# Kernel optimization log

Measured on AMD Instinct MI355X. Metric: run time of the kernel, lower is better.

The kernel has to match this reference:

```python
import jax, jax.numpy as jnp
import numpy as np

CAT_SIZES = [31360, 6807, 18, 94]
TOTAL = int(sum(CAT_SIZES))          # 38279
EMB = 128
N_FIELDS = len(CAT_SIZES)
D_IN = N_FIELDS * EMB                # 512 (num_features is empty)
MLP_DIMS = [2048, 1024, 512]
B = 16384
OFFSETS = np.concatenate([[0], np.cumsum(CAT_SIZES)[:-1]]).astype(np.int32)


def setup_inputs() -> dict:
    key = jax.random.key(0)
    ks = jax.random.split(key, 20)
    # x holds raw per-field category ids stored as float32 (as the torch model expects)
    cols = [jax.random.randint(ks[i], (B,), 0, s) for i, s in enumerate(CAT_SIZES)]
    x = jnp.stack(cols, axis=1).astype(jnp.float32)

    bias = jnp.zeros((1,), jnp.float32)
    fc = jax.random.uniform(ks[4], (TOTAL, 1), dtype=jnp.float32)          # nn.Parameter(torch.rand)
    emb_table = jax.random.normal(ks[5], (TOTAL, EMB), dtype=jnp.float32)  # nn.Embedding default N(0,1)

    dims = [D_IN] + MLP_DIMS + [1]
    params = {}
    for i in range(len(dims) - 1):
        fan_in = dims[i]
        bound = 1.0 / np.sqrt(fan_in)
        params[f"W{i+1}"] = jax.random.uniform(ks[6 + 2 * i], (dims[i], dims[i + 1]), jnp.float32, -bound, bound)
        params[f"b{i+1}"] = jax.random.uniform(ks[7 + 2 * i], (dims[i + 1],), jnp.float32, -bound, bound)

    return dict(x=x, bias=bias, fc=fc, emb_table=emb_table, **params)


def reference(x, bias, fc, emb_table, W1, b1, W2, b2, W3, b3, W4, b4):
    cat = x.astype(jnp.int32)                       # [B, F] raw per-field ids
    b = cat.shape[0]

    # embedding lookup with RAW (un-offset) ids, faithful to the original code
    embed_x = emb_table[cat].reshape(b, -1)          # [B, F*EMB]

    # one_hot(offset ids) @ fc  ==  sum_f fc[offset ids]  (offset ranges disjoint)
    gidx = cat + jnp.asarray(OFFSETS)                # [B, F] global ids
    lin = jnp.sum(fc[gidx, 0], axis=1)               # [B]
    fm_y = bias + lin                                # [B]

    # FM term: embed_x is 2-D, so sum over dim=1 collapses features;
    # the keepdim sum over dim=-1 then collapses the BATCH dim to shape (1,)
    # (a quirk of the original code that we reproduce exactly)
    square_of_sum = jnp.sum(embed_x, axis=1) ** 2    # [B]
    sum_of_square = jnp.sum(embed_x ** 2, axis=1)    # [B]
    fm_y = fm_y + 0.5 * jnp.sum(square_of_sum - sum_of_square, axis=-1, keepdims=True)  # [B]
    fm_y = fm_y[:, None]                             # [B,1]

    # MLP (eval mode: dropout is identity)
    h = embed_x
    for W, bb in ((W1, b1), (W2, b2), (W3, b3)):
        h = jax.nn.relu(h @ W + bb)
    mlp_y = h @ W4 + b4                              # [B,1]

    return jax.nn.sigmoid(fm_y + mlp_y)              # [B,1]
```

## Files before the change

kernel.cpp:

```cpp
#include <hip/hip_runtime.h>
#include <hip/hip_fp8.h>
#include <cstdint>


typedef float f32x4 __attribute__((ext_vector_type(4)));
typedef int i32x4 __attribute__((ext_vector_type(4)));
typedef int i32x8 __attribute__((ext_vector_type(8)));

#define GLOAD16(gptr, lptr)                                                \
  __builtin_amdgcn_global_load_lds(                                        \
      (const __attribute__((address_space(1))) void*)(gptr),               \
      (__attribute__((address_space(3))) void*)(lptr), 16, 0, 0)

__device__ inline uint32_t f2fp4(float v) {
  uint32_t s = (__float_as_uint(v) >> 31) << 3;
  float a = fabsf(v);
  uint32_t m;
  if (a < 0.25f) m = 0;
  else if (a < 0.75f) m = 1;
  else if (a < 1.25f) m = 2;
  else if (a < 1.75f) m = 3;
  else if (a < 2.5f)  m = 4;
  else if (a < 3.5f)  m = 5;
  else if (a < 5.0f)  m = 6;
  else m = 7;
  return s | m;
}

static constexpr size_t OFF_LIN  = 0;
static constexpr size_t OFF_PART = 65536;
static constexpr size_t OFF_ACC  = 98304;
static constexpr size_t OFF_EMB  = 262144;
static constexpr size_t OFF_H1   = OFF_EMB + 8388608ull;
static constexpr size_t OFF_H2   = OFF_H1 + 33554432ull;
static constexpr size_t OFF_W1T  = OFF_H2 + 16777216ull;
static constexpr size_t OFF_W2T  = OFF_W1T + 524288ull;
static constexpr size_t OFF_W3T  = OFF_W2T + 1048576ull;

__global__ void prep(const float* __restrict__ W1, const float* __restrict__ W2,
                     const float* __restrict__ W3, uint8_t* __restrict__ W1T,
                     uint8_t* __restrict__ W2T, uint8_t* __restrict__ W3T,
                     const float* __restrict__ x, const float* __restrict__ fc,
                     const float* __restrict__ emb, uint8_t* __restrict__ ebf,
                     float* __restrict__ lin, float* __restrict__ partials,
                     float* __restrict__ dotacc) {
  __shared__ __align__(16) float smem[32 * 33];
  int blk = blockIdx.x;
  int tid = threadIdx.x;
  if (blk < 3584) {
    const float* W;
    uint8_t* WT;
    int K, N, bx, by;
    if (blk < 1024) {
      W = W1; WT = W1T; K = 512; N = 2048; bx = blk & 63; by = blk >> 6;
    } else if (blk < 3072) {
      int t = blk - 1024;
      W = W2; WT = W2T; K = 2048; N = 1024; bx = t & 31; by = t >> 5;
    } else {
      int t = blk - 3072;
      W = W3; WT = W3T; K = 1024; N = 512; bx = t & 15; by = t >> 4;
    }
    int tx = tid & 31, ty = tid >> 5;
    int n0 = bx * 32, k0 = by * 32;
#pragma unroll
    for (int i = ty; i < 32; i += 8)
      smem[i * 33 + tx] = W[(size_t)(k0 + i) * N + n0 + tx];
    __syncthreads();
    if (tx < 16) {
#pragma unroll
      for (int i = ty; i < 32; i += 8) {
        uint32_t lo = f2fp4(smem[(2 * tx) * 33 + i] * 128.f);
        uint32_t hi = f2fp4(smem[(2 * tx + 1) * 33 + i] * 128.f);
        WT[(size_t)(n0 + i) * (K >> 1) + (k0 >> 1) + tx] =
            (uint8_t)(lo | (hi << 4));
      }
    }
  } else if (blk < 7680) {
    int gb = blk - 3584;
    int wv = tid >> 6, lane = tid & 63;
    int b = gb * 4 + wv;
    int f = lane >> 4;
    int idx = (int)x[b * 4 + f];
    const float* row = emb + (size_t)idx * 128 + (lane & 15) * 8;
    float4 v0 = ((const float4*)row)[0];
    float4 v1 = ((const float4*)row)[1];
    float s = v0.x + v0.y + v0.z + v0.w + v1.x + v1.y + v1.z + v1.w;
    float q = v0.x * v0.x + v0.y * v0.y + v0.z * v0.z + v0.w * v0.w +
              v1.x * v1.x + v1.y * v1.y + v1.z * v1.z + v1.w * v1.w;

    int lo = 0, hi = 0;
    lo = __builtin_amdgcn_cvt_pk_fp8_f32(v0.x, v0.y, lo, false);
    lo = __builtin_amdgcn_cvt_pk_fp8_f32(v0.z, v0.w, lo, true);
    hi = __builtin_amdgcn_cvt_pk_fp8_f32(v1.x, v1.y, hi, false);
    hi = __builtin_amdgcn_cvt_pk_fp8_f32(v1.z, v1.w, hi, true);
    int2 pk = make_int2(lo, hi);
    *(int2*)(ebf + (size_t)b * 512 + lane * 8) = pk;

    float lp = 0.f;
    if ((lane & 15) == 0) {
      int off = (f == 1) ? 31360 : (f == 2) ? 38167 : (f == 3) ? 38185 : 0;
      lp = fc[idx + off];
    }
#pragma unroll
    for (int m = 32; m; m >>= 1) {
      s += __shfl_xor(s, m);
      q += __shfl_xor(q, m);
      lp += __shfl_xor(lp, m);
    }
    float* pt = smem;
    if (lane == 0) {
      lin[b] = lp;
      pt[wv] = s * s - q;
    }
    __syncthreads();
    if (tid == 0) partials[gb] = pt[0] + pt[1] + pt[2] + pt[3];
  } else {
    int zb = blk - 7680;
    ((float4*)dotacc)[zb * 256 + tid] = make_float4(0.f, 0.f, 0.f, 0.f);
  }
}

__global__ __launch_bounds__(256) void gemm_mx_relu(
    const uint8_t* __restrict__ A, const uint8_t* __restrict__ BT,
    const float* __restrict__ bias, uint8_t* __restrict__ C, int K, int N,
    int GX) {
  __shared__ __align__(16) uint8_t As[128][256];
  __shared__ __align__(16) uint8_t Bs[128][128];
  int bid = blockIdx.x;
  int by = (bid & 7) + ((bid >> 3) / GX) * 8;
  int bx = (bid >> 3) & (GX - 1);
  int tid = threadIdx.x;
  int wv = tid >> 6, lane = tid & 63;
  int m0 = by * 128, n0 = bx * 128;
  int mw = (wv >> 1) * 64, nw = (wv & 1) * 64;
  int ml = lane & 15, kg = lane >> 4;
  int Kb2 = K >> 1;
  int arow = lane >> 4;
  int brow = lane >> 3;
  int bcol = ((lane & 7) ^ brow) * 16;

  f32x4 acc[4][4];
#pragma unroll
  for (int i = 0; i < 4; ++i)
#pragma unroll
    for (int j = 0; j < 4; ++j) acc[i][j] = (f32x4){0.f, 0.f, 0.f, 0.f};

  for (int kt = 0; kt < K; kt += 256) {
#pragma unroll
    for (int r = 0; r < 8; ++r) {
      int g = r * 4 + wv;
      int trow = 4 * g + arow;
      int acol = ((lane & 15) ^ (trow & 15)) * 16;
      const uint8_t* ga = A + (size_t)(m0 + trow) * K + kt + acol;
      GLOAD16(ga, &As[4 * g][0]);
    }
#pragma unroll
    for (int r = 0; r < 4; ++r) {
      int g = r * 4 + wv;
      const uint8_t* gb =
          BT + (size_t)(n0 + 8 * g + brow) * Kb2 + (kt >> 1) + bcol;
      GLOAD16(gb, &Bs[8 * g][0]);
    }
    __syncthreads();

    i32x4 z = (i32x4){0, 0, 0, 0};
#pragma unroll
    for (int j = 0; j < 2; ++j) {
      int c0 = 8 * j + 2 * kg;
      int pa0 = (c0 ^ ml) * 16;
      int pa1 = ((c0 + 1) ^ ml) * 16;
      int pb = ((4 * j + kg) ^ (ml & 7)) * 16;
      i32x8 af[4], bfr[4];
#pragma unroll
      for (int t = 0; t < 4; ++t) {
        int ra = mw + t * 16 + ml;
        i32x4 a0 = *(const i32x4*)&As[ra][pa0];
        i32x4 a1 = *(const i32x4*)&As[ra][pa1];
        af[t] = __builtin_shufflevector(a0, a1, 0, 1, 2, 3, 4, 5, 6, 7);
        i32x4 vb = *(const i32x4*)&Bs[nw + t * 16 + ml][pb];
        bfr[t] = __builtin_shufflevector(vb, z, 0, 1, 2, 3, 4, 5, 6, 7);
      }
#pragma unroll
      for (int mt = 0; mt < 4; ++mt)
#pragma unroll
        for (int nt = 0; nt < 4; ++nt)
          acc[mt][nt] = __builtin_amdgcn_mfma_scale_f32_16x16x128_f8f6f4(
              af[mt], bfr[nt], acc[mt][nt],
               0,  4,
              0, 0x7F7F7F7F, 0, 0x78787878);
    }
    __syncthreads();
  }

  int rbase = kg * 4;
#pragma unroll
  for (int nt = 0; nt < 4; ++nt) {
    int col = n0 + nw + nt * 16 + ml;
    float bv = bias[col];
#pragma unroll
    for (int mt = 0; mt < 4; ++mt) {
      int row = m0 + mw + mt * 16 + rbase;
      float v0 = acc[mt][nt][0] + bv, v1 = acc[mt][nt][1] + bv;
      float v2 = acc[mt][nt][2] + bv, v3 = acc[mt][nt][3] + bv;
      v0 = v0 > 0.f ? v0 : 0.f;
      v1 = v1 > 0.f ? v1 : 0.f;
      v2 = v2 > 0.f ? v2 : 0.f;
      v3 = v3 > 0.f ? v3 : 0.f;
      int w01 = __builtin_amdgcn_cvt_pk_fp8_f32(v0, v1, 0, false);
      int w23 = __builtin_amdgcn_cvt_pk_fp8_f32(v2, v3, 0, false);
      C[(size_t)(row + 0) * N + col] = (uint8_t)(w01 & 0xFF);
      C[(size_t)(row + 1) * N + col] = (uint8_t)((w01 >> 8) & 0xFF);
      C[(size_t)(row + 2) * N + col] = (uint8_t)(w23 & 0xFF);
      C[(size_t)(row + 3) * N + col] = (uint8_t)((w23 >> 8) & 0xFF);
    }
  }
}

__global__ __launch_bounds__(256) void gemm_mx_dot(
    const uint8_t* __restrict__ A, const uint8_t* __restrict__ BT,
    const float* __restrict__ bias, const float* __restrict__ W4,
    float* __restrict__ dotacc, int K, int N, int GX) {
  __shared__ __align__(16) uint8_t As[128][256];
  __shared__ __align__(16) uint8_t Bs[128][128];
  int bid = blockIdx.x;
  int by = (bid & 7) + ((bid >> 3) / GX) * 8;
  int bx = (bid >> 3) & (GX - 1);
  int tid = threadIdx.x;
  int wv = tid >> 6, lane = tid & 63;
  int m0 = by * 128, n0 = bx * 128;
  int mw = (wv >> 1) * 64, nw = (wv & 1) * 64;
  int ml = lane & 15, kg = lane >> 4;
  int Kb2 = K >> 1;
  int arow = lane >> 4;
  int brow = lane >> 3;
  int bcol = ((lane & 7) ^ brow) * 16;

  f32x4 acc[4][4];
#pragma unroll
  for (int i = 0; i < 4; ++i)
#pragma unroll
    for (int j = 0; j < 4; ++j) acc[i][j] = (f32x4){0.f, 0.f, 0.f, 0.f};

  for (int kt = 0; kt < K; kt += 256) {
#pragma unroll
    for (int r = 0; r < 8; ++r) {
      int g = r * 4 + wv;
      int trow = 4 * g + arow;
      int acol = ((lane & 15) ^ (trow & 15)) * 16;
      const uint8_t* ga = A + (size_t)(m0 + trow) * K + kt + acol;
      GLOAD16(ga, &As[4 * g][0]);
    }
#pragma unroll
    for (int r = 0; r < 4; ++r) {
      int g = r * 4 + wv;
      const uint8_t* gb =
          BT + (size_t)(n0 + 8 * g + brow) * Kb2 + (kt >> 1) + bcol;
      GLOAD16(gb, &Bs[8 * g][0]);
    }
    __syncthreads();

    i32x4 z = (i32x4){0, 0, 0, 0};
#pragma unroll
    for (int j = 0; j < 2; ++j) {
      int c0 = 8 * j + 2 * kg;
      int pa0 = (c0 ^ ml) * 16;
      int pa1 = ((c0 + 1) ^ ml) * 16;
      int pb = ((4 * j + kg) ^ (ml & 7)) * 16;
      i32x8 af[4], bfr[4];
#pragma unroll
      for (int t = 0; t < 4; ++t) {
        int ra = mw + t * 16 + ml;
        i32x4 a0 = *(const i32x4*)&As[ra][pa0];
        i32x4 a1 = *(const i32x4*)&As[ra][pa1];
        af[t] = __builtin_shufflevector(a0, a1, 0, 1, 2, 3, 4, 5, 6, 7);
        i32x4 vb = *(const i32x4*)&Bs[nw + t * 16 + ml][pb];
        bfr[t] = __builtin_shufflevector(vb, z, 0, 1, 2, 3, 4, 5, 6, 7);
      }
#pragma unroll
      for (int mt = 0; mt < 4; ++mt)
#pragma unroll
        for (int nt = 0; nt < 4; ++nt)
          acc[mt][nt] = __builtin_amdgcn_mfma_scale_f32_16x16x128_f8f6f4(
              af[mt], bfr[nt], acc[mt][nt],
              0, 4, 0, 0x7F7F7F7F, 0, 0x78787878);
    }
    __syncthreads();
  }

  float bv[4], w4v[4];
#pragma unroll
  for (int nt = 0; nt < 4; ++nt) {
    int col = n0 + nw + nt * 16 + ml;
    bv[nt] = bias[col];
    w4v[nt] = W4[col];
  }
  int rbase = kg * 4;
#pragma unroll
  for (int mt = 0; mt < 4; ++mt) {
#pragma unroll
    for (int r = 0; r < 4; ++r) {
      float p = 0.f;
#pragma unroll
      for (int nt = 0; nt < 4; ++nt) {
        float v = acc[mt][nt][r] + bv[nt];
        v = v > 0.f ? v : 0.f;
        p += v * w4v[nt];
      }
#pragma unroll
      for (int m = 1; m < 16; m <<= 1) p += __shfl_xor(p, m);
      if (ml == 0)
        atomicAdd(&dotacc[m0 + mw + mt * 16 + rbase + r], p);
    }
  }
}

__global__ void final_out(const float* __restrict__ part,
                          const float* __restrict__ dotacc,
                          const float* __restrict__ lin,
                          const float* __restrict__ bias,
                          const float* __restrict__ b4,
                          float* __restrict__ out) {
  __shared__ float ps[4];
  int tid = threadIdx.x;
  float v = 0.f;
  for (int i = tid; i < 4096; i += 256) v += part[i];
#pragma unroll
  for (int m = 32; m; m >>= 1) v += __shfl_xor(v, m);
  if ((tid & 63) == 0) ps[tid >> 6] = v;
  __syncthreads();
  float S = ps[0] + ps[1] + ps[2] + ps[3];
  int i = blockIdx.x * 256 + tid;
  float z = dotacc[i] + b4[0] + bias[0] + lin[i] + 0.5f * S;
  out[i] = 1.f / (1.f + expf(-z));
}

extern "C" void kernel_launch(void* const* d_in, const int* in_sizes, int n_in,
                              void* d_out, int out_size, void* d_ws,
                              size_t ws_size, hipStream_t stream) {
  const float* x    = (const float*)d_in[0];
  const float* bias = (const float*)d_in[1];
  const float* fc   = (const float*)d_in[2];
  const float* emb  = (const float*)d_in[3];
  const float* W1   = (const float*)d_in[4];
  const float* b1   = (const float*)d_in[5];
  const float* W2   = (const float*)d_in[6];
  const float* b2   = (const float*)d_in[7];
  const float* W3   = (const float*)d_in[8];
  const float* b3   = (const float*)d_in[9];
  const float* W4   = (const float*)d_in[10];
  const float* b4   = (const float*)d_in[11];
  float* out = (float*)d_out;

  char* ws = (char*)d_ws;
  float* lin    = (float*)(ws + OFF_LIN);
  float* part   = (float*)(ws + OFF_PART);
  float* dacc   = (float*)(ws + OFF_ACC);
  uint8_t* EMBb = (uint8_t*)(ws + OFF_EMB);
  uint8_t* H1   = (uint8_t*)(ws + OFF_H1);
  uint8_t* H2   = (uint8_t*)(ws + OFF_H2);
  uint8_t* W1T  = (uint8_t*)(ws + OFF_W1T);
  uint8_t* W2T  = (uint8_t*)(ws + OFF_W2T);
  uint8_t* W3T  = (uint8_t*)(ws + OFF_W3T);

  prep<<<7696, 256, 0, stream>>>(W1, W2, W3, W1T, W2T, W3T, x, fc, emb, EMBb,
                                 lin, part, dacc);

  gemm_mx_relu<<<2048, 256, 0, stream>>>(EMBb, W1T, b1, H1, 512, 2048, 16);
  gemm_mx_relu<<<1024, 256, 0, stream>>>(H1, W2T, b2, H2, 2048, 1024, 8);
  gemm_mx_dot<<<512, 256, 0, stream>>>(H2, W3T, b3, W4, dacc, 1024, 512, 4);

  final_out<<<64, 256, 0, stream>>>(part, dacc, lin, bias, b4, out);
}
```

Before: 177.1 us.

## Double-buffer LDS tiles with K=128 steps in MX GEMM kernels

Both MX-fp8/fp4 GEMM kernels now use two LDS buffers with a K-step of 128 instead of one buffer with a K-step of 256. The next tile is prefetched with global_load_lds while the current one is consumed, using explicit vmcnt waits and raw barriers in place of __syncthreads. MFMA issue is wrapped in s_setprio. The LDS swizzle patterns are redone for the narrower tiles. This targets load latency that the old single-buffer loop exposed, at the cost of more iterations and barriers per K and reliance on exact vmcnt counting.

```diff
diff --git a/kernel.cpp b/kernel.cpp
--- a/kernel.cpp
+++ b/kernel.cpp
@@ -11,6 +11,9 @@
   __builtin_amdgcn_global_load_lds(                                        \
       (const __attribute__((address_space(1))) void*)(gptr),               \
       (__attribute__((address_space(3))) void*)(lptr), 16, 0, 0)
+
+#define BARRIER() asm volatile("s_barrier" ::: "memory")
+#define WAITVM(n) asm volatile("s_waitcnt vmcnt(" #n ")" ::: "memory")
 
 __device__ inline uint32_t f2fp4(float v) {
   uint32_t s = (__float_as_uint(v) >> 31) << 3;
@@ -124,8 +127,8 @@
     const uint8_t* __restrict__ A, const uint8_t* __restrict__ BT,
     const float* __restrict__ bias, uint8_t* __restrict__ C, int K, int N,
     int GX) {
-  __shared__ __align__(16) uint8_t As[128][256];
-  __shared__ __align__(16) uint8_t Bs[128][128];
+  __shared__ __align__(16) uint8_t As[2][128][128];
+  __shared__ __align__(16) uint8_t Bs[2][128][64];
   int bid = blockIdx.x;
   int by = (bid & 7) + ((bid >> 3) / GX) * 8;
   int bx = (bid >> 3) & (GX - 1);
@@ -135,9 +138,11 @@
   int mw = (wv >> 1) * 64, nw = (wv & 1) * 64;
   int ml = lane & 15, kg = lane >> 4;
   int Kb2 = K >> 1;
-  int arow = lane >> 4;
-  int brow = lane >> 3;
-  int bcol = ((lane & 7) ^ brow) * 16;
+
+  int arow = lane >> 3;
+  int acol = ((lane & 7) ^ arow) * 16;
+  int brow = lane >> 2;
+  int bcol = ((lane & 3) ^ ((lane >> 3) & 3)) * 16;
 
   f32x4 acc[4][4];
 #pragma unroll
@@ -145,63 +150,74 @@
 #pragma unroll
     for (int j = 0; j < 4; ++j) acc[i][j] = (f32x4){0.f, 0.f, 0.f, 0.f};
 
-  for (int kt = 0; kt < K; kt += 256) {
-#pragma unroll
-    for (int r = 0; r < 8; ++r) {
-      int g = r * 4 + wv;
-      int trow = 4 * g + arow;
-      int acol = ((lane & 15) ^ (trow & 15)) * 16;
-      const uint8_t* ga = A + (size_t)(m0 + trow) * K + kt + acol;
-      GLOAD16(ga, &As[4 * g][0]);
-    }
+  int nt = K >> 7;
+
+  auto stage = [&](int buf, int kt) {
 #pragma unroll
     for (int r = 0; r < 4; ++r) {
       int g = r * 4 + wv;
+      const uint8_t* ga = A + (size_t)(m0 + 8 * g + arow) * K + kt + acol;
+      GLOAD16(ga, &As[buf][8 * g][0]);
+    }
+#pragma unroll
+    for (int r = 0; r < 2; ++r) {
+      int g = r * 4 + wv;
       const uint8_t* gb =
-          BT + (size_t)(n0 + 8 * g + brow) * Kb2 + (kt >> 1) + bcol;
-      GLOAD16(gb, &Bs[8 * g][0]);
-    }
-    __syncthreads();
+          BT + (size_t)(n0 + 16 * g + brow) * Kb2 + (kt >> 1) + bcol;
+      GLOAD16(gb, &Bs[buf][16 * g][0]);
+    }
+  };
+
+  int pa0 = ((2 * kg) ^ (ml & 7)) * 16;
+  int pa1 = ((2 * kg + 1) ^ (ml & 7)) * 16;
+  int pb = (kg ^ ((ml >> 1) & 3)) * 16;
+
+  stage(0, 0);
+  int p = 0;
+  for (int t = 0; t < nt; ++t) {
+    if (t + 1 < nt) {
+      stage(p ^ 1, (t + 1) << 7);
+      WAITVM(6);
+    } else {
+      WAITVM(0);
+    }
+    BARRIER();
 
     i32x4 z = (i32x4){0, 0, 0, 0};
-#pragma unroll
-    for (int j = 0; j < 2; ++j) {
-      int c0 = 8 * j + 2 * kg;
-      int pa0 = (c0 ^ ml) * 16;
-      int pa1 = ((c0 + 1) ^ ml) * 16;
-      int pb = ((4 * j + kg) ^ (ml & 7)) * 16;
-      i32x8 af[4], bfr[4];
-#pragma unroll
-      for (int t = 0; t < 4; ++t) {
-        int ra = mw + t * 16 + ml;
-        i32x4 a0 = *(const i32x4*)&As[ra][pa0];
-        i32x4 a1 = *(const i32x4*)&As[ra][pa1];
-        af[t] = __builtin_shufflevector(a0, a1, 0, 1, 2, 3, 4, 5, 6, 7);
-        i32x4 vb = *(const i32x4*)&Bs[nw + t * 16 + ml][pb];
-        bfr[t] = __builtin_shufflevector(vb, z, 0, 1, 2, 3, 4, 5, 6, 7);
-      }
-#pragma unroll
-      for (int mt = 0; mt < 4; ++mt)
-#pragma unroll
-        for (int nt = 0; nt < 4; ++nt)
-          acc[mt][nt] = __builtin_amdgcn_mfma_scale_f32_16x16x128_f8f6f4(
-              af[mt], bfr[nt], acc[mt][nt],
-               0,  4,
-              0, 0x7F7F7F7F, 0, 0x78787878);
-    }
-    __syncthreads();
+    i32x8 af[4], bfr[4];
+#pragma unroll
+    for (int tt = 0; tt < 4; ++tt) {
+      int ra = mw + tt * 16 + ml;
+      i32x4 a0 = *(const i32x4*)&As[p][ra][pa0];
+      i32x4 a1 = *(const i32x4*)&As[p][ra][pa1];
+      af[tt] = __builtin_shufflevector(a0, a1, 0, 1, 2, 3, 4, 5, 6, 7);
+      i32x4 vb = *(const i32x4*)&Bs[p][nw + tt * 16 + ml][pb];
+      bfr[tt] = __builtin_shufflevector(vb, z, 0, 1, 2, 3, 4, 5, 6, 7);
+    }
+    __builtin_amdgcn_s_setprio(1);
+#pragma unroll
+    for (int mt = 0; mt < 4; ++mt)
+#pragma unroll
+      for (int ntt = 0; ntt < 4; ++ntt)
+        acc[mt][ntt] = __builtin_amdgcn_mfma_scale_f32_16x16x128_f8f6f4(
+            af[mt], bfr[ntt], acc[mt][ntt],
+             0,  4,
+            0, 0x7F7F7F7F, 0, 0x78787878);
+    __builtin_amdgcn_s_setprio(0);
+    BARRIER();
+    p ^= 1;
   }
 
   int rbase = kg * 4;
 #pragma unroll
-  for (int nt = 0; nt < 4; ++nt) {
-    int col = n0 + nw + nt * 16 + ml;
+  for (int ntt = 0; ntt < 4; ++ntt) {
+    int col = n0 + nw + ntt * 16 + ml;
     float bv = bias[col];
 #pragma unroll
     for (int mt = 0; mt < 4; ++mt) {
       int row = m0 + mw + mt * 16 + rbase;
-      float v0 = acc[mt][nt][0] + bv, v1 = acc[mt][nt][1] + bv;
-      float v2 = acc[mt][nt][2] + bv, v3 = acc[mt][nt][3] + bv;
+      float v0 = acc[mt][ntt][0] + bv, v1 = acc[mt][ntt][1] + bv;
+      float v2 = acc[mt][ntt][2] + bv, v3 = acc[mt][ntt][3] + bv;
       v0 = v0 > 0.f ? v0 : 0.f;
       v1 = v1 > 0.f ? v1 : 0.f;
       v2 = v2 > 0.f ? v2 : 0.f;
@@ -220,8 +236,8 @@
     const uint8_t* __restrict__ A, const uint8_t* __restrict__ BT,
     const float* __restrict__ bias, const float* __restrict__ W4,
     float* __restrict__ dotacc, int K, int N, int GX) {
-  __shared__ __align__(16) uint8_t As[128][256];
-  __shared__ __align__(16) uint8_t Bs[128][128];
+  __shared__ __align__(16) uint8_t As[2][128][128];
+  __shared__ __align__(16) uint8_t Bs[2][128][64];
   int bid = blockIdx.x;
   int by = (bid & 7) + ((bid >> 3) / GX) * 8;
   int bx = (bid >> 3) & (GX - 1);
@@ -231,9 +247,11 @@
   int mw = (wv >> 1) * 64, nw = (wv & 1) * 64;
   int ml = lane & 15, kg = lane >> 4;
   int Kb2 = K >> 1;
-  int arow = lane >> 4;
-  int brow = lane >> 3;
-  int bcol = ((lane & 7) ^ brow) * 16;
+
+  int arow = lane >> 3;
+  int acol = ((lane & 7) ^ arow) * 16;
+  int brow = lane >> 2;
+  int bcol = ((lane & 3) ^ ((lane >> 3) & 3)) * 16;
 
   f32x4 acc[4][4];
 #pragma unroll
@@ -241,75 +259,86 @@
 #pragma unroll
     for (int j = 0; j < 4; ++j) acc[i][j] = (f32x4){0.f, 0.f, 0.f, 0.f};
 
-  for (int kt = 0; kt < K; kt += 256) {
-#pragma unroll
-    for (int r = 0; r < 8; ++r) {
-      int g = r * 4 + wv;
-      int trow = 4 * g + arow;
-      int acol = ((lane & 15) ^ (trow & 15)) * 16;
-      const uint8_t* ga = A + (size_t)(m0 + trow) * K + kt + acol;
-      GLOAD16(ga, &As[4 * g][0]);
-    }
+  int nt = K >> 7;
+
+  auto stage = [&](int buf, int kt) {
 #pragma unroll
     for (int r = 0; r < 4; ++r) {
       int g = r * 4 + wv;
+      const uint8_t* ga = A + (size_t)(m0 + 8 * g + arow) * K + kt + acol;
+      GLOAD16(ga, &As[buf][8 * g][0]);
+    }
+#pragma unroll
+    for (int r = 0; r < 2; ++r) {
+      int g = r * 4 + wv;
       const uint8_t* gb =
-          BT + (size_t)(n0 + 8 * g + brow) * Kb2 + (kt >> 1) + bcol;
-      GLOAD16(gb, &Bs[8 * g][0]);
-    }
-    __syncthreads();
+          BT + (size_t)(n0 + 16 * g + brow) * Kb2 + (kt >> 1) + bcol;
+      GLOAD16(gb, &Bs[buf][16 * g][0]);
+    }
+  };
+
+  int pa0 = ((2 * kg) ^ (ml & 7)) * 16;
+  int pa1 = ((2 * kg + 1) ^ (ml & 7)) * 16;
+  int pb = (kg ^ ((ml >> 1) & 3)) * 16;
+
+  stage(0, 0);
+  int p = 0;
+  for (int t = 0; t < nt; ++t) {
+    if (t + 1 < nt) {
+      stage(p ^ 1, (t + 1) << 7);
+      WAITVM(6);
+    } else {
+      WAITVM(0);
+    }
+    BARRIER();
 
     i32x4 z = (i32x4){0, 0, 0, 0};
-#pragma unroll
-    for (int j = 0; j < 2; ++j) {
-      int c0 = 8 * j + 2 * kg;
-      int pa0 = (c0 ^ ml) * 16;
-      int pa1 = ((c0 + 1) ^ ml) * 16;
-      int pb = ((4 * j + kg) ^ (ml & 7)) * 16;
-      i32x8 af[4], bfr[4];
-#pragma unroll
-      for (int t = 0; t < 4; ++t) {
-        int ra = mw + t * 16 + ml;
-        i32x4 a0 = *(const i32x4*)&As[ra][pa0];
-        i32x4 a1 = *(const i32x4*)&As[ra][pa1];
-        af[t] = __builtin_shufflevector(a0, a1, 0, 1, 2, 3, 4, 5, 6, 7);
-        i32x4 vb = *(const i32x4*)&Bs[nw + t * 16 + ml][pb];
-        bfr[t] = __builtin_shufflevector(vb, z, 0, 1, 2, 3, 4, 5, 6, 7);
+    i32x8 af[4], bfr[4];
+#pragma unroll
+    for (int tt = 0; tt < 4; ++tt) {
+      int ra = mw + tt * 16 + ml;
+      i32x4 a0 = *(const i32x4*)&As[p][ra][pa0];
+      i32x4 a1 = *(const i32x4*)&As[p][ra][pa1];
+      af[tt] = __builtin_shufflevector(a0, a1, 0, 1, 2, 3, 4, 5, 6, 7);
+      i32x4 vb = *(const i32x4*)&Bs[p][nw + tt * 16 + ml][pb];
+      bfr[tt] = __builtin_shufflevector(vb, z, 0, 1, 2, 3, 4, 5, 6, 7);
+    }
+    __builtin_amdgcn_s_setprio(1);
+#pragma unroll
+    for (int mt = 0; mt < 4; ++mt)
+#pragma unroll
+      for (int ntt = 0; ntt < 4; ++ntt)
+        acc[mt][ntt] = __builtin_amdgcn_mfma_scale_f32_16x16x128_f8f6f4(
+            af[mt], bfr[ntt], acc[mt][ntt],
+            0, 4, 0, 0x7F7F7F7F, 0, 0x78787878);
+    __builtin_amdgcn_s_setprio(0);
+    BARRIER();
+    p ^= 1;
+  }
+
+  float bv[4], w4v[4];
+#pragma unroll
+  for (int ntt = 0; ntt < 4; ++ntt) {
+    int col = n0 + nw + ntt * 16 + ml;
+    bv[ntt] = bias[col];
+    w4v[ntt] = W4[col];
+  }
+  int rbase = kg * 4;
+#pragma unroll
+  for (int mt = 0; mt < 4; ++mt) {
+#pragma unroll
+    for (int r = 0; r < 4; ++r) {
+      float pacc = 0.f;
+#pragma unroll
+      for (int ntt = 0; ntt < 4; ++ntt) {
+        float v = acc[mt][ntt][r] + bv[ntt];
+        v = v > 0.f ? v : 0.f;
+        pacc += v * w4v[ntt];
       }
 #pragma unroll
-      for (int mt = 0; mt < 4; ++mt)
-#pragma unroll
-        for (int nt = 0; nt < 4; ++nt)
-          acc[mt][nt] = __builtin_amdgcn_mfma_scale_f32_16x16x128_f8f6f4(
-              af[mt], bfr[nt], acc[mt][nt],
-              0, 4, 0, 0x7F7F7F7F, 0, 0x78787878);
-    }
-    __syncthreads();
-  }
-
-  float bv[4], w4v[4];
-#pragma unroll
-  for (int nt = 0; nt < 4; ++nt) {
-    int col = n0 + nw + nt * 16 + ml;
-    bv[nt] = bias[col];
-    w4v[nt] = W4[col];
-  }
-  int rbase = kg * 4;
-#pragma unroll
-  for (int mt = 0; mt < 4; ++mt) {
-#pragma unroll
-    for (int r = 0; r < 4; ++r) {
-      float p = 0.f;
-#pragma unroll
-      for (int nt = 0; nt < 4; ++nt) {
-        float v = acc[mt][nt][r] + bv[nt];
-        v = v > 0.f ? v : 0.f;
-        p += v * w4v[nt];
-      }
-#pragma unroll
-      for (int m = 1; m < 16; m <<= 1) p += __shfl_xor(p, m);
+      for (int m = 1; m < 16; m <<= 1) pacc += __shfl_xor(pacc, m);
       if (ml == 0)
-        atomicAdd(&dotacc[m0 + mw + mt * 16 + rbase + r], p);
+        atomicAdd(&dotacc[m0 + mw + mt * 16 + rbase + r], pacc);
     }
   }
 }
```

Result: slower. 181.1 us (+2.3%).
